# Performance work log

Measured on AMD Instinct MI355X. Metric: run time of the kernel, lower is better.

The kernel has to match this reference:

```python
import jax, jax.numpy as jnp
import numpy as np

B, N, E = 128, 1024, 16384
ENTITY, EMB, HID = 100000, 100, 100


def setup_inputs() -> dict:
    key = jax.random.key(0)
    ks = jax.random.split(key, 13)
    s = 0.1  # param init scale
    return {
        "neighbors": jax.random.randint(ks[0], (B, N), 0, ENTITY),
        "adj_row": jax.random.randint(ks[1], (B, E), 0, N),
        "adj_col": jax.random.randint(ks[2], (B, E), 0, N),
        "adj_val": jax.random.uniform(ks[3], (B, E), jnp.float32),
        "emb_table": jax.random.normal(ks[4], (ENTITY, EMB), jnp.float32) * s,
        "gcn_w": jax.random.normal(ks[5], (EMB, HID), jnp.float32) * s,
        "gcn_b": jax.random.normal(ks[6], (HID,), jnp.float32) * s,
        "w_ih": jax.random.normal(ks[7], (3 * HID, HID), jnp.float32) * s,
        "w_hh": jax.random.normal(ks[8], (3 * HID, HID), jnp.float32) * s,
        "b_ih": jax.random.normal(ks[9], (3 * HID,), jnp.float32) * s,
        "b_hh": jax.random.normal(ks[10], (3 * HID,), jnp.float32) * s,
        "fc1_w": jax.random.normal(ks[11], (HID, HID), jnp.float32) * s,
        "fc1_b": jax.random.normal(ks[12], (HID,), jnp.float32) * s,
    }


def reference(neighbors, adj_row, adj_col, adj_val, emb_table,
              gcn_w, gcn_b, w_ih, w_hh, b_ih, b_hh, fc1_w, fc1_b):
    n_nodes = neighbors.shape[1]
    # Embedding lookup: [B, N, EMB]
    x = emb_table[neighbors]
    # GCN layer: support = X @ W, then sparse adj @ support, then + bias
    support = jnp.einsum('bne,eh->bnh', x, gcn_w)  # [B, N, HID]

    def spmm(row, col, val, sup):
        # out[r] += val * sup[col]  (per-sample sparse aggregation)
        return jax.ops.segment_sum(val[:, None] * sup[col], row,
                                   num_segments=n_nodes)

    seq = jax.vmap(spmm)(adj_row, adj_col, adj_val, support) + gcn_b  # [B,N,HID]

    # GRU over node sequence (PyTorch gate order: r, z, n)
    def gru_step(h, x_t):
        gx = x_t @ w_ih.T + b_ih
        gh = h @ w_hh.T + b_hh
        xr, xz, xn = jnp.split(gx, 3, axis=-1)
        hr, hz, hn = jnp.split(gh, 3, axis=-1)
        r = jax.nn.sigmoid(xr + hr)
        z = jax.nn.sigmoid(xz + hz)
        n = jnp.tanh(xn + r * hn)
        h_new = (1.0 - z) * n + z * h
        return h_new, None

    h0 = jnp.zeros((seq.shape[0], w_hh.shape[1]), seq.dtype)
    h, _ = jax.lax.scan(gru_step, h0, seq.transpose(1, 0, 2))  # final hidden [B,HID]

    # h.permute(1,0,2) -> [B, 1, HID], then relu(fc1(.))
    return jax.nn.relu(h[:, None, :] @ fc1_w.T + fc1_b)
```

## Files before the change

### kernel.cpp

```cpp
#include <hip/hip_runtime.h>
#include <hip/hip_bf16.h>


typedef unsigned int u32;
typedef float f2 __attribute__((ext_vector_type(2)));

__device__ __forceinline__ float bflo(u32 u) {
    union { u32 i; float f; } v; v.i = u << 16; return v.f;
}
__device__ __forceinline__ float bfhi(u32 u) {
    union { u32 i; float f; } v; v.i = u & 0xffff0000u; return v.f;
}
__device__ __forceinline__ u32 f2bf1(float f) {
    union { float f; u32 u; } v; v.f = f;
    return (v.u + 0x7fffu + ((v.u >> 16) & 1u)) >> 16;
}
__device__ __forceinline__ u32 packbf(float a, float b) {
    return f2bf1(a) | (f2bf1(b) << 16);
}
__device__ __forceinline__ float sigm(float x) { return 1.f / (1.f + __expf(-x)); }
__device__ __forceinline__ float tanh_fast(float x) {
    float e = __expf(2.f * x);
    return 1.f - 2.f / (e + 1.f);
}

__global__ __launch_bounds__(256, 2)
void gcn_kernel(const int* __restrict__ nb, const float* __restrict__ emb,
                const float* __restrict__ w, u32* __restrict__ support)
{
    __shared__ float wl[10000];
    for (int i = threadIdx.x; i < 10000; i += 256) wl[i] = w[i];
    __syncthreads();

    const int n = blockIdx.x * 256 + threadIdx.x;
    const long long row = nb[n];
    const float4* __restrict__ xr = (const float4*)(emb + row * 100);

    float acc[100];
#pragma unroll
    for (int h = 0; h < 100; ++h) acc[h] = 0.f;

    for (int kk = 0; kk < 25; ++kk) {
        const float4 xv = xr[kk];
        const float xs[4] = { xv.x, xv.y, xv.z, xv.w };
#pragma unroll
        for (int q = 0; q < 4; ++q) {
            const float* wrow = &wl[(kk * 4 + q) * 100];
            const float xq = xs[q];
#pragma unroll
            for (int h4 = 0; h4 < 25; ++h4) {
                const float4 w4 = *(const float4*)(wrow + h4 * 4);
                acc[h4*4+0] = fmaf(xq, w4.x, acc[h4*4+0]);
                acc[h4*4+1] = fmaf(xq, w4.y, acc[h4*4+1]);
                acc[h4*4+2] = fmaf(xq, w4.z, acc[h4*4+2]);
                acc[h4*4+3] = fmaf(xq, w4.w, acc[h4*4+3]);
            }
        }
    }

    u32* __restrict__ o = support + (size_t)n * 50;
#pragma unroll
    for (int i = 0; i < 50; ++i) o[i] = packbf(acc[2*i], acc[2*i+1]);
}

__global__ __launch_bounds__(256, 2)
void csr_build(const int* __restrict__ arow, const int* __restrict__ acol,
               const float* __restrict__ aval,
               int* __restrict__ offs, int2* __restrict__ csr)
{
    __shared__ int cnt[1024];
    __shared__ int part[256];
    __shared__ int offl[1024];

    const int b   = blockIdx.x;
    const int tid = threadIdx.x;
    const int*   rw = arow + b * 16384;
    const int*   cl = acol + b * 16384;
    const float* vl = aval + b * 16384;

    for (int i = tid; i < 1024; i += 256) cnt[i] = 0;
    __syncthreads();
    for (int e = tid; e < 16384; e += 256) atomicAdd(&cnt[rw[e]], 1);
    __syncthreads();

    int c[4]; int s = 0;
#pragma unroll
    for (int q = 0; q < 4; ++q) { c[q] = cnt[tid * 4 + q]; s += c[q]; }
    part[tid] = s;
    __syncthreads();
    for (int off = 1; off < 256; off <<= 1) {
        int v = (tid >= off) ? part[tid - off] : 0;
        __syncthreads();
        part[tid] += v;
        __syncthreads();
    }
    int run = part[tid] - s;
#pragma unroll
    for (int q = 0; q < 4; ++q) { offl[tid * 4 + q] = run; run += c[q]; }
    __syncthreads();

    for (int i = tid; i < 1024; i += 256) offs[b * 1025 + i] = offl[i];
    if (tid == 0) offs[b * 1025 + 1024] = 16384;

    int2* cs = csr + (size_t)b * 16384;
    for (int e = tid; e < 16384; e += 256) {
        const int r   = rw[e];
        const int pos = atomicAdd(&offl[r], 1);
        int2 cv; cv.x = cl[e]; cv.y = __float_as_int(vl[e]);
        cs[pos] = cv;
    }
}

__global__ __launch_bounds__(256, 4)
void spmm_agg(const int* __restrict__ offs, const int2* __restrict__ csr,
              const u32* __restrict__ support,
              const float* __restrict__ gcn_b, u32* __restrict__ seq)
{
    const int b    = blockIdx.y;
    const int lr   = threadIdx.x / 50;
    const int lane = threadIdx.x % 50;
    const int r    = blockIdx.x * 5 + lr;
    if (lr >= 5 || r >= 1024) return;

    const int e0 = offs[b * 1025 + r];
    const int e1 = offs[b * 1025 + r + 1];
    const int2* __restrict__ cs = csr + (size_t)b * 16384;
    const u32* __restrict__ supb = support + (size_t)b * 1024 * 50;

    float a0 = 0.f, a1 = 0.f;
    for (int e = e0; e < e1; ++e) {
        const int2 cv = cs[e];
        const float v = __int_as_float(cv.y);
        const u32 u = supb[(size_t)cv.x * 50 + lane];
        a0 = fmaf(v, bflo(u), a0);
        a1 = fmaf(v, bfhi(u), a1);
    }
    a0 += gcn_b[2 * lane];
    a1 += gcn_b[2 * lane + 1];
    seq[((size_t)b * 1024 + r) * 50 + lane] = packbf(a0, a1);
}

__global__ __launch_bounds__(256, 2)
void gx_gemm0(const u32* __restrict__ seq, const float* __restrict__ w_ih,
              const float* __restrict__ b_ih, u32* __restrict__ gxW,
              int c0, int ctl, int CT)
{
    __shared__ float wl[10000];
    const int g    = blockIdx.x % 3;
    const int tile = blockIdx.x / 3;
    const int tid  = threadIdx.x;

    for (int i = tid; i < 10000; i += 256)
        wl[(i % 100) * 100 + (i / 100)] = w_ih[g * 10000 + i];
    __syncthreads();

    const int m = tile * 256 + tid;
    const int b = m >> ctl;
    const int t = m & (CT - 1);
    const uint2* sr2 = (const uint2*)(seq + ((size_t)b * 1024 + c0 + t) * 50);

    float acc[100];
    const float4* bi4 = (const float4*)(b_ih + g * 100);
#pragma unroll
    for (int j4 = 0; j4 < 25; ++j4) {
        const float4 bv = bi4[j4];
        acc[j4*4+0] = bv.x; acc[j4*4+1] = bv.y; acc[j4*4+2] = bv.z; acc[j4*4+3] = bv.w;
    }

    for (int kk = 0; kk < 25; ++kk) {
        const uint2 up = sr2[kk];
        const float xs[4] = { bflo(up.x), bfhi(up.x), bflo(up.y), bfhi(up.y) };
#pragma unroll
        for (int q = 0; q < 4; ++q) {
            const float* wrow = &wl[(kk * 4 + q) * 100];
            const float xq = xs[q];
#pragma unroll
            for (int j4 = 0; j4 < 25; ++j4) {
                const float4 w4 = *(const float4*)(wrow + j4 * 4);
                acc[j4*4+0] = fmaf(xq, w4.x, acc[j4*4+0]);
                acc[j4*4+1] = fmaf(xq, w4.y, acc[j4*4+1]);
                acc[j4*4+2] = fmaf(xq, w4.z, acc[j4*4+2]);
                acc[j4*4+3] = fmaf(xq, w4.w, acc[j4*4+3]);
            }
        }
    }

    u32* og = gxW + (size_t)m * 150 + g * 50;
#pragma unroll
    for (int i = 0; i < 50; ++i) og[i] = packbf(acc[2*i], acc[2*i+1]);
}

__global__ __launch_bounds__(640, 1)
void gru_v3(const u32* __restrict__ gxR, size_t sampStride,
            const float* __restrict__ w_hh, const float* __restrict__ b_hh,
            float* __restrict__ hg, const float* __restrict__ fc1_w,
            const float* __restrict__ fc1_b, float* __restrict__ out,
            int first, int last, int CT)
{
    __shared__ float h[100];
    __shared__ float ps[600];

    const int tid  = threadIdx.x;
    const int samp = blockIdx.x;
    const int p    = tid / 320;
    const int r    = tid - p * 320;
    const bool rowAct = (r < 300);
    const int NG   = 13 - p;

    f2 wk[26];
    if (rowAct) {
        const float* wrow = w_hh + (size_t)r * 100;
#pragma unroll
        for (int i = 0; i < 13; ++i) {
            if (i < NG) {
                const int q = 2 * i + p;
                const float4 wv = *(const float4*)(wrow + 4 * q);
                wk[2*i]   = (f2){wv.x, wv.y};
                wk[2*i+1] = (f2){wv.z, wv.w};
            }
        }
    }

    float bhr = 0.f, bhz = 0.f, bhn = 0.f;
    if (tid < 100) {
        bhr = b_hh[tid]; bhz = b_hh[100 + tid]; bhn = b_hh[200 + tid];
        h[tid] = first ? 0.f : hg[samp * 100 + tid];
    }
    __syncthreads();

    const int odd = tid & 1;
    const u32* gp = gxR + (size_t)samp * sampStride + (tid >> 1);
    u32 a0 = 0, a1 = 0, a2 = 0, b0 = 0, b1 = 0, b2 = 0;
    if (tid < 100) {
        a0 = gp[0];   a1 = gp[50];  a2 = gp[100];
        b0 = gp[150]; b1 = gp[200]; b2 = gp[250];
    }

    auto stepf = [&](int t, u32& x0, u32& x1, u32& x2) {
        float sum = 0.f;
        if (rowAct) {
            f2 acc0 = {0.f, 0.f}, acc1 = {0.f, 0.f};
#pragma unroll
            for (int i = 0; i < 13; ++i) {
                if (i < NG) {
                    const int q = 2 * i + p;
                    const float4 hv = *(const float4*)(&h[4 * q]);
                    acc0 += wk[2*i]   * (f2){hv.x, hv.y};
                    acc1 += wk[2*i+1] * (f2){hv.z, hv.w};
                }
            }
            sum = (acc0.x + acc0.y) + (acc1.x + acc1.y);
        }
        const u32 c0 = x0, c1 = x1, c2 = x2;
        if (tid < 100 && t + 2 < CT) {
            const u32* q2 = gp + (size_t)(t + 2) * 150;
            x0 = q2[0]; x1 = q2[50]; x2 = q2[100];
        }
        if (rowAct) ps[p * 300 + r] = sum;
        __syncthreads();
        if (tid < 100) {
            const float ghr = ps[tid]       + ps[300 + tid] + bhr;
            const float ghz = ps[100 + tid] + ps[400 + tid] + bhz;
            const float ghn = ps[200 + tid] + ps[500 + tid] + bhn;
            const float gxr = odd ? bfhi(c0) : bflo(c0);
            const float gxz = odd ? bfhi(c1) : bflo(c1);
            const float gxn = odd ? bfhi(c2) : bflo(c2);
            const float rg = sigm(gxr + ghr);
            const float zg = sigm(gxz + ghz);
            const float ng = tanh_fast(gxn + rg * ghn);
            h[tid] = (1.f - zg) * ng + zg * h[tid];
        }
        __syncthreads();
    };

    for (int t = 0; t < CT; t += 2) {
        stepf(t,     a0, a1, a2);
        stepf(t + 1, b0, b1, b2);
    }

    if (tid < 100) {
        hg[samp * 100 + tid] = h[tid];
        if (last) {
            const float4* fw = (const float4*)(fc1_w + (size_t)tid * 100);
            float s0 = 0.f, s1 = 0.f, s2 = 0.f, s3 = 0.f;
#pragma unroll
            for (int kk = 0; kk < 25; ++kk) {
                const float4 wv = fw[kk];
                const float4 hv = *(const float4*)(&h[kk * 4]);
                s0 = fmaf(wv.x, hv.x, s0);
                s1 = fmaf(wv.y, hv.y, s1);
                s2 = fmaf(wv.z, hv.z, s2);
                s3 = fmaf(wv.w, hv.w, s3);
            }
            const float s = (s0 + s1) + (s2 + s3) + fc1_b[tid];
            out[samp * 100 + tid] = fmaxf(s, 0.f);
        }
    }
}

extern "C" void kernel_launch(void* const* d_in, const int* in_sizes, int n_in,
                              void* d_out, int out_size, void* d_ws, size_t ws_size,
                              hipStream_t stream)
{
    const int*   neighbors = (const int*)  d_in[0];
    const int*   adj_row   = (const int*)  d_in[1];
    const int*   adj_col   = (const int*)  d_in[2];
    const float* adj_val   = (const float*)d_in[3];
    const float* emb       = (const float*)d_in[4];
    const float* gcn_w     = (const float*)d_in[5];
    const float* gcn_b     = (const float*)d_in[6];
    const float* w_ih      = (const float*)d_in[7];
    const float* w_hh      = (const float*)d_in[8];
    const float* b_ih      = (const float*)d_in[9];
    const float* b_hh      = (const float*)d_in[10];
    const float* fc1_w     = (const float*)d_in[11];
    const float* fc1_b     = (const float*)d_in[12];
    float* out = (float*)d_out;

    char* ws = (char*)d_ws;
    const size_t seq_bytes     = (size_t)128 * 1024 * 50 * 4;
    const size_t hg_bytes      = 128 * 100 * 4;
    const size_t support_bytes = (size_t)128 * 1024 * 50 * 4;
    const size_t offs_bytes    = (size_t)128 * 1025 * 4;

    u32*   seq = (u32*)ws;
    float* hg  = (float*)(ws + seq_bytes);
    char*  rest = ws + seq_bytes + hg_bytes;
    const size_t rest_avail = ws_size - seq_bytes - hg_bytes;

    u32*  support = (u32*)rest;
    int*  offs    = (int*)(rest + support_bytes);
    int2* csr     = (int2*)(rest + support_bytes + offs_bytes);

    gcn_kernel<<<512, 256, 0, stream>>>(neighbors, emb, gcn_w, support);
    csr_build<<<128, 256, 0, stream>>>(adj_row, adj_col, adj_val, offs, csr);
    spmm_agg<<<dim3(205, 128), 256, 0, stream>>>(offs, csr, support, gcn_b, seq);

    const size_t gx_full = (size_t)128 * 1024 * 150 * 4;
    u32* gx = (u32*)rest;

    if (rest_avail >= gx_full) {
        gx_gemm0<<<1536, 256, 0, stream>>>(seq, w_ih, b_ih, gx, 0, 10, 1024);
        gru_v3<<<128, 640, 0, stream>>>(gx, (size_t)1024 * 150, w_hh, b_hh, hg,
                                        fc1_w, fc1_b, out, 1, 1, 1024);
    } else {
        int CT = 512, ctl = 9;
        while (CT > 8 && (size_t)128 * CT * 150 * 4 > rest_avail) { CT >>= 1; --ctl; }
        const int nch = 1024 / CT;
        for (int c = 0; c < nch; ++c) {
            gx_gemm0<<<3 * (128 * CT / 256), 256, 0, stream>>>(seq, w_ih, b_ih, gx,
                                                               c * CT, ctl, CT);
            gru_v3<<<128, 640, 0, stream>>>(gx, (size_t)CT * 150, w_hh, b_hh, hg,
                                            fc1_w, fc1_b, out,
                                            (c == 0) ? 1 : 0, (c == nch - 1) ? 1 : 0, CT);
        }
    }
}
```

Before: 1.323 ms.

## Restructure GRU step so each lane pair owns all three gates of a unit

The GRU recurrence kernel now runs 256 threads per sample. Each pair of lanes computes the r, z and n dot products for one hidden unit, keeping 78 weight pairs in registers, and combines the two halves with a cross-lane shuffle instead of a shared partial-sum buffer. The hidden state is double-buffered in shared memory, which removes one of the two block barriers per timestep and the separate gate-combine phase. In exchange it needs more registers per thread and does more serial FMA work per lane on each step.

```diff
diff --git a/kernel.cpp b/kernel.cpp
--- a/kernel.cpp
+++ b/kernel.cpp
@@ -190,87 +190,95 @@
     for (int i = 0; i < 50; ++i) og[i] = packbf(acc[2*i], acc[2*i+1]);
 }
 
-__global__ __launch_bounds__(640, 1)
-void gru_v3(const u32* __restrict__ gxR, size_t sampStride,
+__global__ __launch_bounds__(256, 1)
+void gru_v4(const u32* __restrict__ gxR, size_t sampStride,
             const float* __restrict__ w_hh, const float* __restrict__ b_hh,
             float* __restrict__ hg, const float* __restrict__ fc1_w,
             const float* __restrict__ fc1_b, float* __restrict__ out,
             int first, int last, int CT)
 {
-    __shared__ float h[100];
-    __shared__ float ps[600];
+    __shared__ float h[2][100];
 
     const int tid  = threadIdx.x;
     const int samp = blockIdx.x;
-    const int p    = tid / 320;
-    const int r    = tid - p * 320;
-    const bool rowAct = (r < 300);
-    const int NG   = 13 - p;
-
-    f2 wk[26];
-    if (rowAct) {
-        const float* wrow = w_hh + (size_t)r * 100;
+    const int wave = tid >> 6;
+    const int lane = tid & 63;
+    const bool act = (lane < 50);
+    const int  j   = wave * 25 + (lane >> 1);
+    const int  p   = lane & 1;
+    const int  jodd = j & 1;
+
+    f2 wr[26], wz[26], wn[26];
+    float bhr = 0.f, bhz = 0.f, bhn = 0.f, hcur = 0.f;
+    if (act) {
+        const float* rrow = w_hh + (size_t)j * 100;
+        const float* zrow = w_hh + (size_t)(100 + j) * 100;
+        const float* nrow = w_hh + (size_t)(200 + j) * 100;
 #pragma unroll
         for (int i = 0; i < 13; ++i) {
-            if (i < NG) {
-                const int q = 2 * i + p;
-                const float4 wv = *(const float4*)(wrow + 4 * q);
-                wk[2*i]   = (f2){wv.x, wv.y};
-                wk[2*i+1] = (f2){wv.z, wv.w};
-            }
-        }
-    }
-
-    float bhr = 0.f, bhz = 0.f, bhn = 0.f;
-    if (tid < 100) {
-        bhr = b_hh[tid]; bhz = b_hh[100 + tid]; bhn = b_hh[200 + tid];
-        h[tid] = first ? 0.f : hg[samp * 100 + tid];
-    }
-    __syncthreads();
-
-    const int odd = tid & 1;
-    const u32* gp = gxR + (size_t)samp * sampStride + (tid >> 1);
+            const int q = 2 * i + p;
+            if (q < 25) {
+                const float4 a = *(const float4*)(rrow + 4 * q);
+                wr[2*i] = (f2){a.x, a.y}; wr[2*i+1] = (f2){a.z, a.w};
+                const float4 b = *(const float4*)(zrow + 4 * q);
+                wz[2*i] = (f2){b.x, b.y}; wz[2*i+1] = (f2){b.z, b.w};
+                const float4 c = *(const float4*)(nrow + 4 * q);
+                wn[2*i] = (f2){c.x, c.y}; wn[2*i+1] = (f2){c.z, c.w};
+            }
+        }
+        bhr = b_hh[j]; bhz = b_hh[100 + j]; bhn = b_hh[200 + j];
+        hcur = first ? 0.f : hg[samp * 100 + j];
+        if (!p) h[0][j] = hcur;
+    }
+    __syncthreads();
+
+    const u32* gp = gxR + (size_t)samp * sampStride + (j >> 1);
     u32 a0 = 0, a1 = 0, a2 = 0, b0 = 0, b1 = 0, b2 = 0;
-    if (tid < 100) {
+    if (act) {
         a0 = gp[0];   a1 = gp[50];  a2 = gp[100];
         b0 = gp[150]; b1 = gp[200]; b2 = gp[250];
     }
+    int par = 0;
 
     auto stepf = [&](int t, u32& x0, u32& x1, u32& x2) {
-        float sum = 0.f;
-        if (rowAct) {
-            f2 acc0 = {0.f, 0.f}, acc1 = {0.f, 0.f};
+        f2 ar = {0.f,0.f}, az = {0.f,0.f}, an = {0.f,0.f};
+        if (act) {
 #pragma unroll
             for (int i = 0; i < 13; ++i) {
-                if (i < NG) {
-                    const int q = 2 * i + p;
-                    const float4 hv = *(const float4*)(&h[4 * q]);
-                    acc0 += wk[2*i]   * (f2){hv.x, hv.y};
-                    acc1 += wk[2*i+1] * (f2){hv.z, hv.w};
+                const int q = 2 * i + p;
+                if (q < 25) {
+                    const float4 hv = *(const float4*)(&h[par][4 * q]);
+                    const f2 hA = (f2){hv.x, hv.y};
+                    const f2 hB = (f2){hv.z, hv.w};
+                    ar += wr[2*i] * hA; ar += wr[2*i+1] * hB;
+                    az += wz[2*i] * hA; az += wz[2*i+1] * hB;
+                    an += wn[2*i] * hA; an += wn[2*i+1] * hB;
                 }
             }
-            sum = (acc0.x + acc0.y) + (acc1.x + acc1.y);
         }
         const u32 c0 = x0, c1 = x1, c2 = x2;
-        if (tid < 100 && t + 2 < CT) {
+        if (act && t + 2 < CT) {
             const u32* q2 = gp + (size_t)(t + 2) * 150;
             x0 = q2[0]; x1 = q2[50]; x2 = q2[100];
         }
-        if (rowAct) ps[p * 300 + r] = sum;
+        if (act) {
+            float sr = ar.x + ar.y;
+            float sz = az.x + az.y;
+            float sn = an.x + an.y;
+            sr += __shfl_xor(sr, 1);
+            sz += __shfl_xor(sz, 1);
+            sn += __shfl_xor(sn, 1);
+            const float gxr = jodd ? bfhi(c0) : bflo(c0);
+            const float gxz = jodd ? bfhi(c1) : bflo(c1);
+            const float gxn = jodd ? bfhi(c2) : bflo(c2);
+            const float rg = sigm(gxr + sr + bhr);
+            const float zg = sigm(gxz + sz + bhz);
+            const float ng = tanh_fast(gxn + rg * (sn + bhn));
+            hcur = (1.f - zg) * ng + zg * hcur;
+            if (!p) h[par ^ 1][j] = hcur;
+        }
         __syncthreads();
-        if (tid < 100) {
-            const float ghr = ps[tid]       + ps[300 + tid] + bhr;
-            const float ghz = ps[100 + tid] + ps[400 + tid] + bhz;
-            const float ghn = ps[200 + tid] + ps[500 + tid] + bhn;
-            const float gxr = odd ? bfhi(c0) : bflo(c0);
-            const float gxz = odd ? bfhi(c1) : bflo(c1);
-            const float gxn = odd ? bfhi(c2) : bflo(c2);
-            const float rg = sigm(gxr + ghr);
-            const float zg = sigm(gxz + ghz);
-            const float ng = tanh_fast(gxn + rg * ghn);
-            h[tid] = (1.f - zg) * ng + zg * h[tid];
-        }
-        __syncthreads();
+        par ^= 1;
     };
 
     for (int t = 0; t < CT; t += 2) {
@@ -278,22 +286,22 @@
         stepf(t + 1, b0, b1, b2);
     }
 
-    if (tid < 100) {
-        hg[samp * 100 + tid] = h[tid];
+    if (act && !p) {
+        hg[samp * 100 + j] = hcur;
         if (last) {
-            const float4* fw = (const float4*)(fc1_w + (size_t)tid * 100);
+            const float4* fw = (const float4*)(fc1_w + (size_t)j * 100);
             float s0 = 0.f, s1 = 0.f, s2 = 0.f, s3 = 0.f;
 #pragma unroll
             for (int kk = 0; kk < 25; ++kk) {
                 const float4 wv = fw[kk];
-                const float4 hv = *(const float4*)(&h[kk * 4]);
+                const float4 hv = *(const float4*)(&h[par][kk * 4]);
                 s0 = fmaf(wv.x, hv.x, s0);
                 s1 = fmaf(wv.y, hv.y, s1);
                 s2 = fmaf(wv.z, hv.z, s2);
                 s3 = fmaf(wv.w, hv.w, s3);
             }
-            const float s = (s0 + s1) + (s2 + s3) + fc1_b[tid];
-            out[samp * 100 + tid] = fmaxf(s, 0.f);
+            const float s = (s0 + s1) + (s2 + s3) + fc1_b[j];
+            out[samp * 100 + j] = fmaxf(s, 0.f);
         }
     }
 }
@@ -341,7 +349,7 @@
 
     if (rest_avail >= gx_full) {
         gx_gemm0<<<1536, 256, 0, stream>>>(seq, w_ih, b_ih, gx, 0, 10, 1024);
-        gru_v3<<<128, 640, 0, stream>>>(gx, (size_t)1024 * 150, w_hh, b_hh, hg,
+        gru_v4<<<128, 256, 0, stream>>>(gx, (size_t)1024 * 150, w_hh, b_hh, hg,
                                         fc1_w, fc1_b, out, 1, 1, 1024);
     } else {
         int CT = 512, ctl = 9;
@@ -350,7 +358,7 @@
         for (int c = 0; c < nch; ++c) {
             gx_gemm0<<<3 * (128 * CT / 256), 256, 0, stream>>>(seq, w_ih, b_ih, gx,
                                                                c * CT, ctl, CT);
-            gru_v3<<<128, 640, 0, stream>>>(gx, (size_t)CT * 150, w_hh, b_hh, hg,
+            gru_v4<<<128, 256, 0, stream>>>(gx, (size_t)CT * 150, w_hh, b_hh, hg,
                                             fc1_w, fc1_b, out,
                                             (c == 0) ? 1 : 0, (c == nch - 1) ? 1 : 0, CT);
         }
```

Result: slower. 1.423 ms (+7.6%).

## Batch GRU samples per block and compute recurrent matmul with bf16 MFMA

Applied to the files above, without the earlier changes.

Replaces the per-sample GRU kernel with one that packs 8 samples per block and computes the hidden-to-gate product with bf16 16x16x32 MFMA instructions, keeping w_hh fragments in registers and h in a double-buffered LDS tile. This cuts the per-step latency of the serial recurrence and halves barriers per step. It lowers recurrent precision to bf16 for weights and hidden state and uses far fewer blocks. Also adds a missing barrier in the CSR build.

```diff
diff --git a/kernel.cpp b/kernel.cpp
--- a/kernel.cpp
+++ b/kernel.cpp
@@ -3,7 +3,8 @@
 
 
 typedef unsigned int u32;
-typedef float f2 __attribute__((ext_vector_type(2)));
+typedef short short8 __attribute__((ext_vector_type(8)));
+typedef float f32x4 __attribute__((ext_vector_type(4)));
 
 __device__ __forceinline__ float bflo(u32 u) {
     union { u32 i; float f; } v; v.i = u << 16; return v.f;
@@ -101,6 +102,7 @@
 
     for (int i = tid; i < 1024; i += 256) offs[b * 1025 + i] = offl[i];
     if (tid == 0) offs[b * 1025 + 1024] = 16384;
+    __syncthreads();
 
     int2* cs = csr + (size_t)b * 16384;
     for (int e = tid; e < 16384; e += 256) {
@@ -190,110 +192,149 @@
     for (int i = 0; i < 50; ++i) og[i] = packbf(acc[2*i], acc[2*i+1]);
 }
 
-__global__ __launch_bounds__(640, 1)
-void gru_v3(const u32* __restrict__ gxR, size_t sampStride,
-            const float* __restrict__ w_hh, const float* __restrict__ b_hh,
-            float* __restrict__ hg, const float* __restrict__ fc1_w,
-            const float* __restrict__ fc1_b, float* __restrict__ out,
-            int first, int last, int CT)
-{
-    __shared__ float h[100];
-    __shared__ float ps[600];
+__global__ __attribute__((amdgpu_waves_per_eu(1, 2))) __launch_bounds__(448, 1)
+void gru_mfma(const u32* __restrict__ gxR, int CT,
+              const float* __restrict__ w_hh, const float* __restrict__ b_hh,
+              float* __restrict__ hg, const float* __restrict__ fc1_w,
+              const float* __restrict__ fc1_b, float* __restrict__ out,
+              int first, int last)
+{
+    __shared__ unsigned short hA[2][16][136];
 
     const int tid  = threadIdx.x;
-    const int samp = blockIdx.x;
-    const int p    = tid / 320;
-    const int r    = tid - p * 320;
-    const bool rowAct = (r < 300);
-    const int NG   = 13 - p;
-
-    f2 wk[26];
-    if (rowAct) {
-        const float* wrow = w_hh + (size_t)r * 100;
-#pragma unroll
-        for (int i = 0; i < 13; ++i) {
-            if (i < NG) {
-                const int q = 2 * i + p;
-                const float4 wv = *(const float4*)(wrow + 4 * q);
-                wk[2*i]   = (f2){wv.x, wv.y};
-                wk[2*i+1] = (f2){wv.z, wv.w};
-            }
-        }
-    }
-
-    float bhr = 0.f, bhz = 0.f, bhn = 0.f;
-    if (tid < 100) {
-        bhr = b_hh[tid]; bhz = b_hh[100 + tid]; bhn = b_hh[200 + tid];
-        h[tid] = first ? 0.f : hg[samp * 100 + tid];
-    }
-    __syncthreads();
-
-    const int odd = tid & 1;
-    const u32* gp = gxR + (size_t)samp * sampStride + (tid >> 1);
-    u32 a0 = 0, a1 = 0, a2 = 0, b0 = 0, b1 = 0, b2 = 0;
-    if (tid < 100) {
-        a0 = gp[0];   a1 = gp[50];  a2 = gp[100];
-        b0 = gp[150]; b1 = gp[200]; b2 = gp[250];
-    }
-
-    auto stepf = [&](int t, u32& x0, u32& x1, u32& x2) {
-        float sum = 0.f;
-        if (rowAct) {
-            f2 acc0 = {0.f, 0.f}, acc1 = {0.f, 0.f};
-#pragma unroll
-            for (int i = 0; i < 13; ++i) {
-                if (i < NG) {
-                    const int q = 2 * i + p;
-                    const float4 hv = *(const float4*)(&h[4 * q]);
-                    acc0 += wk[2*i]   * (f2){hv.x, hv.y};
-                    acc1 += wk[2*i+1] * (f2){hv.z, hv.w};
-                }
-            }
-            sum = (acc0.x + acc0.y) + (acc1.x + acc1.y);
-        }
-        const u32 c0 = x0, c1 = x1, c2 = x2;
-        if (tid < 100 && t + 2 < CT) {
-            const u32* q2 = gp + (size_t)(t + 2) * 150;
-            x0 = q2[0]; x1 = q2[50]; x2 = q2[100];
-        }
-        if (rowAct) ps[p * 300 + r] = sum;
+    const int wave = tid >> 6;
+    const int lane = tid & 63;
+    const int col  = lane & 15;
+    const int quad = lane >> 4;
+    const int u    = wave * 16 + col;
+    const int uc   = (u < 100) ? u : 0;
+    const int s0   = blockIdx.x * 8;
+    const int sl   = quad * 4;
+    const bool epi = (quad < 2) && (u < 100);
+    const int odd  = u & 1;
+
+    for (int i = tid; i < 2 * 16 * 136; i += 448) ((unsigned short*)hA)[i] = 0;
+
+    short8 bfr[3][4];
+#pragma unroll
+    for (int g = 0; g < 3; ++g)
+#pragma unroll
+        for (int ki = 0; ki < 4; ++ki) {
+            short8 v;
+#pragma unroll
+            for (int j = 0; j < 8; ++j) {
+                const int k = ki * 32 + quad * 8 + j;
+                const float wv = (u < 100 && k < 100)
+                               ? w_hh[(size_t)(g * 100 + u) * 100 + k] : 0.f;
+                v[j] = (short)f2bf1(wv);
+            }
+            bfr[g][ki] = v;
+        }
+    float bh0 = b_hh[uc], bh1 = b_hh[100 + uc], bh2 = b_hh[200 + uc];
+
+    float h_old[4] = {0.f, 0.f, 0.f, 0.f};
+    if (epi && !first) {
+#pragma unroll
+        for (int r = 0; r < 4; ++r) h_old[r] = hg[(s0 + sl + r) * 100 + u];
+    }
+    __syncthreads();
+    if (epi) {
+#pragma unroll
+        for (int r = 0; r < 4; ++r)
+            hA[0][sl + r][u] = (unsigned short)f2bf1(h_old[r]);
+    }
+    __syncthreads();
+
+    const u32* gp[4];
+#pragma unroll
+    for (int r = 0; r < 4; ++r) {
+        const int sg = (s0 + sl + r < 128) ? (s0 + sl + r) : 0;
+        gp[r] = gxR + (size_t)sg * CT * 150 + (uc >> 1);
+    }
+
+    u32 pfA[12], pfB[12];
+#pragma unroll
+    for (int i = 0; i < 12; ++i) { pfA[i] = 0; pfB[i] = 0; }
+    if (epi) {
+#pragma unroll
+        for (int r = 0; r < 4; ++r)
+#pragma unroll
+            for (int g = 0; g < 3; ++g) {
+                pfA[r*3+g] = gp[r][g * 50];
+                if (CT > 1) pfB[r*3+g] = gp[r][150 + g * 50];
+            }
+    }
+    int par = 0;
+
+    auto stepf = [&](int t, u32* pf) {
+        short8 a0 = *(const short8*)&hA[par][col][0  + quad * 8];
+        short8 a1 = *(const short8*)&hA[par][col][32 + quad * 8];
+        short8 a2 = *(const short8*)&hA[par][col][64 + quad * 8];
+        short8 a3 = *(const short8*)&hA[par][col][96 + quad * 8];
+
+        f32x4 accr = {0.f,0.f,0.f,0.f}, accz = {0.f,0.f,0.f,0.f}, accn = {0.f,0.f,0.f,0.f};
+        accr = __builtin_amdgcn_mfma_f32_16x16x32_bf16(a0, bfr[0][0], accr, 0,0,0);
+        accz = __builtin_amdgcn_mfma_f32_16x16x32_bf16(a0, bfr[1][0], accz, 0,0,0);
+        accn = __builtin_amdgcn_mfma_f32_16x16x32_bf16(a0, bfr[2][0], accn, 0,0,0);
+        accr = __builtin_amdgcn_mfma_f32_16x16x32_bf16(a1, bfr[0][1], accr, 0,0,0);
+        accz = __builtin_amdgcn_mfma_f32_16x16x32_bf16(a1, bfr[1][1], accz, 0,0,0);
+        accn = __builtin_amdgcn_mfma_f32_16x16x32_bf16(a1, bfr[2][1], accn, 0,0,0);
+        accr = __builtin_amdgcn_mfma_f32_16x16x32_bf16(a2, bfr[0][2], accr, 0,0,0);
+        accz = __builtin_amdgcn_mfma_f32_16x16x32_bf16(a2, bfr[1][2], accz, 0,0,0);
+        accn = __builtin_amdgcn_mfma_f32_16x16x32_bf16(a2, bfr[2][2], accn, 0,0,0);
+        accr = __builtin_amdgcn_mfma_f32_16x16x32_bf16(a3, bfr[0][3], accr, 0,0,0);
+        accz = __builtin_amdgcn_mfma_f32_16x16x32_bf16(a3, bfr[1][3], accz, 0,0,0);
+        accn = __builtin_amdgcn_mfma_f32_16x16x32_bf16(a3, bfr[2][3], accn, 0,0,0);
+
+        u32 c[12];
+#pragma unroll
+        for (int i = 0; i < 12; ++i) c[i] = pf[i];
+        if (epi && t + 2 < CT) {
+#pragma unroll
+            for (int r = 0; r < 4; ++r)
+#pragma unroll
+                for (int g = 0; g < 3; ++g)
+                    pf[r*3+g] = gp[r][(size_t)(t + 2) * 150 + g * 50];
+        }
+
+        if (epi) {
+#pragma unroll
+            for (int r = 0; r < 4; ++r) {
+                const float gxr = odd ? bfhi(c[r*3+0]) : bflo(c[r*3+0]);
+                const float gxz = odd ? bfhi(c[r*3+1]) : bflo(c[r*3+1]);
+                const float gxn = odd ? bfhi(c[r*3+2]) : bflo(c[r*3+2]);
+                const float rg = sigm(gxr + accr[r] + bh0);
+                const float zg = sigm(gxz + accz[r] + bh1);
+                const float ng = tanh_fast(gxn + rg * (accn[r] + bh2));
+                h_old[r] = (1.f - zg) * ng + zg * h_old[r];
+                hA[par ^ 1][sl + r][u] = (unsigned short)f2bf1(h_old[r]);
+            }
+        }
         __syncthreads();
-        if (tid < 100) {
-            const float ghr = ps[tid]       + ps[300 + tid] + bhr;
-            const float ghz = ps[100 + tid] + ps[400 + tid] + bhz;
-            const float ghn = ps[200 + tid] + ps[500 + tid] + bhn;
-            const float gxr = odd ? bfhi(c0) : bflo(c0);
-            const float gxz = odd ? bfhi(c1) : bflo(c1);
-            const float gxn = odd ? bfhi(c2) : bflo(c2);
-            const float rg = sigm(gxr + ghr);
-            const float zg = sigm(gxz + ghz);
-            const float ng = tanh_fast(gxn + rg * ghn);
-            h[tid] = (1.f - zg) * ng + zg * h[tid];
-        }
-        __syncthreads();
+        par ^= 1;
     };
 
     for (int t = 0; t < CT; t += 2) {
-        stepf(t,     a0, a1, a2);
-        stepf(t + 1, b0, b1, b2);
-    }
-
-    if (tid < 100) {
-        hg[samp * 100 + tid] = h[tid];
-        if (last) {
-            const float4* fw = (const float4*)(fc1_w + (size_t)tid * 100);
-            float s0 = 0.f, s1 = 0.f, s2 = 0.f, s3 = 0.f;
-#pragma unroll
-            for (int kk = 0; kk < 25; ++kk) {
-                const float4 wv = fw[kk];
-                const float4 hv = *(const float4*)(&h[kk * 4]);
-                s0 = fmaf(wv.x, hv.x, s0);
-                s1 = fmaf(wv.y, hv.y, s1);
-                s2 = fmaf(wv.z, hv.z, s2);
-                s3 = fmaf(wv.w, hv.w, s3);
-            }
-            const float s = (s0 + s1) + (s2 + s3) + fc1_b[tid];
-            out[samp * 100 + tid] = fmaxf(s, 0.f);
+        stepf(t,     pfA);
+        stepf(t + 1, pfB);
+    }
+
+    if (epi) {
+#pragma unroll
+        for (int r = 0; r < 4; ++r) hg[(s0 + sl + r) * 100 + u] = h_old[r];
+    }
+
+    if (last) {
+        for (int idx = tid; idx < 800; idx += 448) {
+            const int s = idx / 100, j = idx % 100;
+            const float* fw = fc1_w + (size_t)j * 100;
+            const u32* hr = (const u32*)&hA[par][s][0];
+            float acc = fc1_b[j];
+            for (int k2 = 0; k2 < 50; ++k2) {
+                const u32 hv = hr[k2];
+                acc += fw[2*k2] * bflo(hv) + fw[2*k2+1] * bfhi(hv);
+            }
+            out[(s0 + s) * 100 + j] = fmaxf(acc, 0.f);
         }
     }
 }
@@ -341,8 +382,8 @@
 
     if (rest_avail >= gx_full) {
         gx_gemm0<<<1536, 256, 0, stream>>>(seq, w_ih, b_ih, gx, 0, 10, 1024);
-        gru_v3<<<128, 640, 0, stream>>>(gx, (size_t)1024 * 150, w_hh, b_hh, hg,
-                                        fc1_w, fc1_b, out, 1, 1, 1024);
+        gru_mfma<<<16, 448, 0, stream>>>(gx, 1024, w_hh, b_hh, hg,
+                                         fc1_w, fc1_b, out, 1, 1);
     } else {
         int CT = 512, ctl = 9;
         while (CT > 8 && (size_t)128 * CT * 150 * 4 > rest_avail) { CT >>= 1; --ctl; }
@@ -350,9 +391,9 @@
         for (int c = 0; c < nch; ++c) {
             gx_gemm0<<<3 * (128 * CT / 256), 256, 0, stream>>>(seq, w_ih, b_ih, gx,
                                                                c * CT, ctl, CT);
-            gru_v3<<<128, 640, 0, stream>>>(gx, (size_t)CT * 150, w_hh, b_hh, hg,
-                                            fc1_w, fc1_b, out,
-                                            (c == 0) ? 1 : 0, (c == nch - 1) ? 1 : 0, CT);
-        }
-    }
-}
+            gru_mfma<<<16, 448, 0, stream>>>(gx, CT, w_hh, b_hh, hg,
+                                             fc1_w, fc1_b, out,
+                                             (c == 0) ? 1 : 0, (c == nch - 1) ? 1 : 0);
+        }
+    }
+}
```

Result: slower. 1.952 ms (+47.6%).
